# Kernel optimization log

Measured on AMD Instinct MI355X. Metric: run time of the kernel, lower is better.

Reference implementation:

```python
import jax, jax.numpy as jnp
import numpy as np

H = 12       # heads
D = 768      # hidden size
DH = D // H  # head dim = 64
SCALE = 1.0 / jnp.sqrt(jnp.float32(DH))
LN_EPS = 1e-3  # keras LayerNormalization default epsilon


def setup_inputs() -> dict:
    key = jax.random.key(0)
    ks = jax.random.split(key, 8)
    B, L = 16, 512
    s = 0.02  # truncated-normal-ish init scale
    return {
        "x": jax.random.normal(ks[0], (B, L, D), jnp.float32),
        "mask": jnp.ones((B, L), jnp.int32),
        "Wq": jax.random.normal(ks[1], (D, D), jnp.float32) * s,
        "bq": jnp.zeros((D,), jnp.float32),
        "Wk": jax.random.normal(ks[2], (D, D), jnp.float32) * s,
        "bk": jnp.zeros((D,), jnp.float32),
        "Wv": jax.random.normal(ks[3], (D, D), jnp.float32) * s,
        "bv": jnp.zeros((D,), jnp.float32),
        "Wo": jax.random.normal(ks[4], (D, D), jnp.float32) * s,
        "bo": jnp.zeros((D,), jnp.float32),
        "gamma": jnp.ones((D,), jnp.float32),
        "beta": jnp.zeros((D,), jnp.float32),
    }


def reference(x, mask, Wq, bq, Wk, bk, Wv, bv, Wo, bo, gamma, beta):
    B, L, _ = x.shape
    # QKV projections, split into heads: [B, L, H, DH]
    q = (x @ Wq + bq).reshape(B, L, H, DH)
    k = (x @ Wk + bk).reshape(B, L, H, DH)
    v = (x @ Wv + bv).reshape(B, L, H, DH)
    # scaled dot-product scores: [B, H, Lq, Lk]
    scores = jnp.einsum('bqhd,bkhd->bhqk', q, k) * SCALE
    # key-side padding mask (mask==0 -> -inf)
    neg = jnp.float32(-1e9)
    scores = jnp.where(mask[:, None, None, :] > 0, scores, neg)
    p = jax.nn.softmax(scores, axis=-1)
    # dropout rate fixed to 0.0 -> identity
    ctx = jnp.einsum('bhqk,bkhd->bqhd', p, v).reshape(B, L, D)
    attn_out = ctx @ Wo + bo
    # residual + LayerNorm (keras default eps=1e-3)
    y = x + attn_out
    mu = jnp.mean(y, axis=-1, keepdims=True)
    var = jnp.mean(jnp.square(y - mu), axis=-1, keepdims=True)
    return gamma * (y - mu) * jax.lax.rsqrt(var + LN_EPS) + beta
```

## Files before the change

### kernel.cpp

```cpp
#include <hip/hip_runtime.h>
#include <math.h>

#define NH 12
#define DMODEL 768
#define DHEAD 64
#define BATCH 16
#define SEQ 512
#define NTOK (BATCH*SEQ)
#define ATTN_SCALE 0.125f
#define LN_EPS 1e-3f
#define PADB 72
#define KITERS (DMODEL/64)

typedef __attribute__((ext_vector_type(8))) short  bf16x8;
typedef __attribute__((ext_vector_type(8))) unsigned short ushort8;
typedef __attribute__((ext_vector_type(4))) float  f32x4;

__device__ __forceinline__ unsigned short f2bf(float f) {
    unsigned int u = __float_as_uint(f);
    unsigned int r = (u + 0x7fffu + ((u >> 16) & 1u)) >> 16;
    return (unsigned short)r;
}
__device__ __forceinline__ float bf2f(unsigned short h) {
    return __uint_as_float(((unsigned int)h) << 16);
}

__device__ __forceinline__ void async_copy16(const void* g, void* l) {
    __builtin_amdgcn_global_load_lds((const __attribute__((address_space(1))) void*)g,
                                     (__attribute__((address_space(3))) void*)l,
                                     16, 0, 0);
}

__global__ __launch_bounds__(256) void prep_kernel(
    const float* __restrict__ x,
    const float* __restrict__ Wq, const float* __restrict__ Wk,
    const float* __restrict__ Wv, const float* __restrict__ Wo,
    unsigned short* __restrict__ xb,
    unsigned short* __restrict__ tq, unsigned short* __restrict__ tk,
    unsigned short* __restrict__ tv, unsigned short* __restrict__ to_)
{
    __shared__ float tile[32][33];
    const int bid = blockIdx.x;
    const int tid = threadIdx.x;

    if (bid < 6144) {
        int i = (bid * 256 + tid) * 4;
        const float4 v = *(const float4*)(x + i);
        unsigned long long pack =
              (unsigned long long)f2bf(v.x)
            | ((unsigned long long)f2bf(v.y) << 16)
            | ((unsigned long long)f2bf(v.z) << 32)
            | ((unsigned long long)f2bf(v.w) << 48);
        *(unsigned long long*)(xb + i) = pack;
        return;
    }

    const int t   = bid - 6144;
    const int zz  = t / 576;
    const int rem = t % 576;
    const float* W = (zz == 0) ? Wq : (zz == 1) ? Wk : (zz == 2) ? Wv : Wo;
    unsigned short* T = (zz == 0) ? tq : (zz == 1) ? tk : (zz == 2) ? tv : to_;

    const int bx = (rem / 24) * 32;
    const int by = (rem % 24) * 32;
    const int tx = tid & 31, ty = tid >> 5;

    #pragma unroll
    for (int i = 0; i < 32; i += 8)
        tile[ty + i][tx] = W[(size_t)(bx + ty + i) * DMODEL + by + tx];
    __syncthreads();
    #pragma unroll
    for (int i = 0; i < 32; i += 8)
        T[(size_t)(by + ty + i) * DMODEL + bx + tx] = f2bf(tile[tx][ty + i]);
}

__global__ __launch_bounds__(256, 4) void mfma_gemm_qkv(
    const unsigned short* __restrict__ xb,
    const unsigned short* __restrict__ wt0, const unsigned short* __restrict__ wt1,
    const unsigned short* __restrict__ wt2,
    const float* __restrict__ b0, const float* __restrict__ b1, const float* __restrict__ b2,
    unsigned short* __restrict__ o0, unsigned short* __restrict__ o1,
    unsigned short* __restrict__ o2)
{
    __shared__ __align__(16) unsigned short As[128 * 64];
    __shared__ __align__(16) unsigned short Bs[128 * 64];

    const int zz = blockIdx.z;
    const unsigned short* Wt = (zz == 0) ? wt0 : (zz == 1) ? wt1 : wt2;
    const float* bias        = (zz == 0) ? b0  : (zz == 1) ? b1  : b2;
    unsigned short* out      = (zz == 0) ? o0  : (zz == 1) ? o1  : o2;

    const int tid  = threadIdx.x;
    const int lane = tid & 63;
    const int w    = tid >> 6;
    const int wm   = w >> 1, wn = w & 1;
    const int m0   = blockIdx.x * 128;
    const int n0   = blockIdx.y * 128;
    const int quad = lane >> 4;
    const int l16  = lane & 15;

    const int rloc = lane >> 3;
    const int csw  = (lane & 7) ^ rloc;
    int rowS[4];
    #pragma unroll
    for (int ii = 0; ii < 4; ++ii) rowS[ii] = (4 * w + ii) * 8 + rloc;

    const int p0 = ((quad ^ (l16 & 7)) * 8);

    f32x4 acc[4][4] = {};

    for (int kb = 0; kb < KITERS; ++kb) {
        const int k0 = kb * 64;
        #pragma unroll
        for (int ii = 0; ii < 4; ++ii) {
            async_copy16(xb + (size_t)(m0 + rowS[ii]) * DMODEL + k0 + csw * 8,
                         As + (4 * w + ii) * 512);
            async_copy16(Wt + (size_t)(n0 + rowS[ii]) * DMODEL + k0 + csw * 8,
                         Bs + (4 * w + ii) * 512);
        }
        __syncthreads();

        #pragma unroll
        for (int ks = 0; ks < 2; ++ks) {
            const int po = p0 ^ (ks * 32);
            bf16x8 a[4], b[4];
            #pragma unroll
            for (int mi = 0; mi < 4; ++mi)
                a[mi] = *(const bf16x8*)&As[(wm * 64 + mi * 16 + l16) * 64 + po];
            #pragma unroll
            for (int ni = 0; ni < 4; ++ni)
                b[ni] = *(const bf16x8*)&Bs[(wn * 64 + ni * 16 + l16) * 64 + po];
            #pragma unroll
            for (int mi = 0; mi < 4; ++mi)
                #pragma unroll
                for (int ni = 0; ni < 4; ++ni)
                    acc[mi][ni] = __builtin_amdgcn_mfma_f32_16x16x32_bf16(a[mi], b[ni], acc[mi][ni], 0, 0, 0);
        }
        __syncthreads();
    }

    if (zz == 2) {
        #pragma unroll
        for (int ni = 0; ni < 4; ++ni) {
            const int ncol = n0 + wn * 64 + ni * 16 + l16;
            const int h = ncol >> 6, dh = ncol & 63;
            const float bv = bias[ncol];
            #pragma unroll
            for (int mi = 0; mi < 4; ++mi) {
                const int mbase = m0 + wm * 64 + mi * 16 + quad * 4;
                const int bi = mbase >> 9, l = mbase & 511;
                unsigned long long pack = 0;
                #pragma unroll
                for (int r = 0; r < 4; ++r)
                    pack |= (unsigned long long)f2bf(acc[mi][ni][r] + bv) << (16 * r);
                *(unsigned long long*)(out + ((size_t)((bi * NH + h) * DHEAD + dh)) * SEQ + l) = pack;
            }
        }
    } else {
        #pragma unroll
        for (int ni = 0; ni < 4; ++ni) {
            const int ncol = n0 + wn * 64 + ni * 16 + l16;
            const int h = ncol >> 6, dh = ncol & 63;
            const float bv = bias[ncol];
            #pragma unroll
            for (int mi = 0; mi < 4; ++mi) {
                const int mbase = m0 + wm * 64 + mi * 16 + quad * 4;
                #pragma unroll
                for (int r = 0; r < 4; ++r) {
                    const int t = mbase + r;
                    const int bi = t >> 9, l = t & 511;
                    out[(size_t)((bi * NH + h) * SEQ + l) * DHEAD + dh] = f2bf(acc[mi][ni][r] + bv);
                }
            }
        }
    }
}

__global__ __launch_bounds__(256, 4) void mfma_gemm_oproj(
    const unsigned short* __restrict__ ctxb, const unsigned short* __restrict__ wto,
    const float* __restrict__ bo, const float* __restrict__ x,
    float* __restrict__ y)
{
    __shared__ __align__(16) unsigned short As[128 * 64];
    __shared__ __align__(16) unsigned short Bs[128 * 64];

    const int tid  = threadIdx.x;
    const int lane = tid & 63;
    const int w    = tid >> 6;
    const int wm   = w >> 1, wn = w & 1;
    const int m0   = blockIdx.x * 128;
    const int n0   = blockIdx.y * 128;
    const int quad = lane >> 4;
    const int l16  = lane & 15;

    const int rloc = lane >> 3;
    const int csw  = (lane & 7) ^ rloc;
    int rowS[4];
    #pragma unroll
    for (int ii = 0; ii < 4; ++ii) rowS[ii] = (4 * w + ii) * 8 + rloc;
    const int p0 = ((quad ^ (l16 & 7)) * 8);

    f32x4 acc[4][4] = {};

    for (int kb = 0; kb < KITERS; ++kb) {
        const int k0 = kb * 64;
        #pragma unroll
        for (int ii = 0; ii < 4; ++ii) {
            async_copy16(ctxb + (size_t)(m0 + rowS[ii]) * DMODEL + k0 + csw * 8,
                         As + (4 * w + ii) * 512);
            async_copy16(wto  + (size_t)(n0 + rowS[ii]) * DMODEL + k0 + csw * 8,
                         Bs + (4 * w + ii) * 512);
        }
        __syncthreads();

        #pragma unroll
        for (int ks = 0; ks < 2; ++ks) {
            const int po = p0 ^ (ks * 32);
            bf16x8 a[4], b[4];
            #pragma unroll
            for (int mi = 0; mi < 4; ++mi)
                a[mi] = *(const bf16x8*)&As[(wm * 64 + mi * 16 + l16) * 64 + po];
            #pragma unroll
            for (int ni = 0; ni < 4; ++ni)
                b[ni] = *(const bf16x8*)&Bs[(wn * 64 + ni * 16 + l16) * 64 + po];
            #pragma unroll
            for (int mi = 0; mi < 4; ++mi)
                #pragma unroll
                for (int ni = 0; ni < 4; ++ni)
                    acc[mi][ni] = __builtin_amdgcn_mfma_f32_16x16x32_bf16(a[mi], b[ni], acc[mi][ni], 0, 0, 0);
        }
        __syncthreads();
    }

    #pragma unroll
    for (int ni = 0; ni < 4; ++ni) {
        const int ncol = n0 + wn * 64 + ni * 16 + l16;
        const float bv = bo[ncol];
        #pragma unroll
        for (int mi = 0; mi < 4; ++mi) {
            const int mbase = m0 + wm * 64 + mi * 16 + quad * 4;
            #pragma unroll
            for (int r = 0; r < 4; ++r) {
                const size_t idx = (size_t)(mbase + r) * DMODEL + ncol;
                y[idx] = acc[mi][ni][r] + bv + x[idx];
            }
        }
    }
}

__global__ __launch_bounds__(256) void attn_mfma_kernel(
    const unsigned short* __restrict__ q, const unsigned short* __restrict__ k,
    const unsigned short* __restrict__ vt, const int* __restrict__ mask,
    unsigned short* __restrict__ ctxb)
{
    __shared__ __align__(16) unsigned short Ks[64 * PADB];
    __shared__ __align__(16) unsigned short Vs[64 * PADB];
    __shared__ __align__(16) unsigned short QP[128 * PADB];
    __shared__ float maskF[64];

    const int tid  = threadIdx.x;
    const int lane = tid & 63;
    const int w    = tid >> 6;
    const int quad = lane >> 4;
    const int l16  = lane & 15;
    const int q0   = blockIdx.x * 128;
    const int h    = blockIdx.y;
    const int b    = blockIdx.z;

    const unsigned short* qp  = q  + ((size_t)(b * NH + h) * SEQ + q0) * DHEAD;
    const unsigned short* kp  = k  + (size_t)(b * NH + h) * SEQ * DHEAD;
    const unsigned short* vtp = vt + (size_t)(b * NH + h) * DHEAD * SEQ;

    #pragma unroll
    for (int i = 0; i < 4; ++i) {
        int idx = tid * 8 + 2048 * i;
        *(ushort8*)&QP[(idx >> 6) * PADB + (idx & 63)] = *(const ushort8*)(qp + idx);
    }
    __syncthreads();

    bf16x8 aQ[2][2];
    #pragma unroll
    for (int mi = 0; mi < 2; ++mi)
        #pragma unroll
        for (int kb = 0; kb < 2; ++kb)
            aQ[mi][kb] = *(const bf16x8*)&QP[(w * 32 + mi * 16 + l16) * PADB + kb * 32 + quad * 8];

    bf16x8 ones;
    #pragma unroll
    for (int j = 0; j < 8; ++j) ones[j] = (short)0x3F80;

    float m_st[2][4], l_st[2][4];
    #pragma unroll
    for (int mi = 0; mi < 2; ++mi)
        #pragma unroll
        for (int r = 0; r < 4; ++r) { m_st[mi][r] = -1e30f; l_st[mi][r] = 0.f; }
    f32x4 o[2][4] = {};
    const f32x4 zf = {0.f, 0.f, 0.f, 0.f};

    for (int kt = 0; kt < SEQ; kt += 64) {
        __syncthreads();
        #pragma unroll
        for (int i = 0; i < 2; ++i) {
            int idx = tid * 8 + 2048 * i;
            int r = idx >> 6, c = idx & 63;
            *(ushort8*)&Ks[r * PADB + c] = *(const ushort8*)(kp + (size_t)kt * DHEAD + idx);
            *(ushort8*)&Vs[r * PADB + c] = *(const ushort8*)(vtp + (size_t)r * SEQ + kt + c);
        }
        if (tid < 64) maskF[tid] = (mask[b * SEQ + kt + tid] > 0) ? 0.f : -1e9f;
        __syncthreads();

        f32x4 s[2][4];
        float mk[4];
        #pragma unroll
        for (int ni = 0; ni < 4; ++ni) {
            bf16x8 bK0 = *(const bf16x8*)&Ks[(ni * 16 + l16) * PADB + quad * 8];
            bf16x8 bK1 = *(const bf16x8*)&Ks[(ni * 16 + l16) * PADB + 32 + quad * 8];
            mk[ni] = maskF[ni * 16 + l16];
            #pragma unroll
            for (int mi = 0; mi < 2; ++mi) {
                f32x4 t0 = __builtin_amdgcn_mfma_f32_16x16x32_bf16(aQ[mi][0], bK0, zf, 0, 0, 0);
                s[mi][ni] = __builtin_amdgcn_mfma_f32_16x16x32_bf16(aQ[mi][1], bK1, t0, 0, 0, 0);
            }
        }

        float alpha[2][4];
        #pragma unroll
        for (int mi = 0; mi < 2; ++mi) {
            #pragma unroll
            for (int r = 0; r < 4; ++r) {
                float mx = -3e38f;
                #pragma unroll
                for (int ni = 0; ni < 4; ++ni) {
                    float sv = s[mi][ni][r] * ATTN_SCALE + mk[ni];
                    s[mi][ni][r] = sv;
                    mx = fmaxf(mx, sv);
                }
                mx = fmaxf(mx, __shfl_xor(mx, 1));
                mx = fmaxf(mx, __shfl_xor(mx, 2));
                mx = fmaxf(mx, __shfl_xor(mx, 4));
                mx = fmaxf(mx, __shfl_xor(mx, 8));
                float mo = m_st[mi][r];
                float mn = fmaxf(mo, mx);
                float al = __expf(mo - mn);
                m_st[mi][r] = mn;
                l_st[mi][r] *= al;
                alpha[mi][r] = al;
            }
        }

        #pragma unroll
        for (int mi = 0; mi < 2; ++mi)
            #pragma unroll
            for (int ni = 0; ni < 4; ++ni)
                #pragma unroll
                for (int r = 0; r < 4; ++r)
                    QP[(w * 32 + mi * 16 + quad * 4 + r) * PADB + ni * 16 + l16]
                        = f2bf(__expf(s[mi][ni][r] - m_st[mi][r]));
        #pragma unroll
        for (int mi = 0; mi < 2; ++mi)
            #pragma unroll
            for (int ni = 0; ni < 4; ++ni)
                #pragma unroll
                for (int r = 0; r < 4; ++r)
                    o[mi][ni][r] *= alpha[mi][r];

        bf16x8 aP[2][2];
        #pragma unroll
        for (int mi = 0; mi < 2; ++mi)
            #pragma unroll
            for (int kb = 0; kb < 2; ++kb)
                aP[mi][kb] = *(const bf16x8*)&QP[(w * 32 + mi * 16 + l16) * PADB + kb * 32 + quad * 8];

        f32x4 rs[2];
        #pragma unroll
        for (int mi = 0; mi < 2; ++mi) {
            f32x4 t0 = __builtin_amdgcn_mfma_f32_16x16x32_bf16(aP[mi][0], ones, zf, 0, 0, 0);
            rs[mi] = __builtin_amdgcn_mfma_f32_16x16x32_bf16(aP[mi][1], ones, t0, 0, 0, 0);
        }

        #pragma unroll
        for (int ni = 0; ni < 4; ++ni) {
            bf16x8 bV0 = *(const bf16x8*)&Vs[(ni * 16 + l16) * PADB + quad * 8];
            bf16x8 bV1 = *(const bf16x8*)&Vs[(ni * 16 + l16) * PADB + 32 + quad * 8];
            #pragma unroll
            for (int mi = 0; mi < 2; ++mi) {
                o[mi][ni] = __builtin_amdgcn_mfma_f32_16x16x32_bf16(aP[mi][0], bV0, o[mi][ni], 0, 0, 0);
                o[mi][ni] = __builtin_amdgcn_mfma_f32_16x16x32_bf16(aP[mi][1], bV1, o[mi][ni], 0, 0, 0);
            }
        }
        #pragma unroll
        for (int mi = 0; mi < 2; ++mi)
            #pragma unroll
            for (int r = 0; r < 4; ++r)
                l_st[mi][r] += rs[mi][r];
    }

    #pragma unroll
    for (int mi = 0; mi < 2; ++mi)
        #pragma unroll
        for (int r = 0; r < 4; ++r) {
            float inv = 1.f / l_st[mi][r];
            int tok = q0 + w * 32 + mi * 16 + quad * 4 + r;
            #pragma unroll
            for (int ni = 0; ni < 4; ++ni)
                ctxb[(size_t)(b * SEQ + tok) * DMODEL + h * DHEAD + ni * 16 + l16]
                    = f2bf(o[mi][ni][r] * inv);
        }
}

__global__ __launch_bounds__(256) void ln_kernel(
    const float* __restrict__ y, const float* __restrict__ gamma,
    const float* __restrict__ beta, float* __restrict__ out)
{
    const int t   = blockIdx.x;
    const int tid = threadIdx.x;
    const float* row = y + (size_t)t * DMODEL;

    float vals[3];
    float s = 0.f, s2 = 0.f;
    #pragma unroll
    for (int i = 0; i < 3; ++i) {
        float vv = row[tid + 256 * i];
        vals[i] = vv;
        s  += vv;
        s2 += vv * vv;
    }
    #pragma unroll
    for (int off = 32; off > 0; off >>= 1) {
        s  += __shfl_down(s,  off);
        s2 += __shfl_down(s2, off);
    }
    __shared__ float rbuf[8];
    int w = tid >> 6;
    if ((tid & 63) == 0) { rbuf[w] = s; rbuf[4 + w] = s2; }
    __syncthreads();
    float ts  = rbuf[0] + rbuf[1] + rbuf[2] + rbuf[3];
    float ts2 = rbuf[4] + rbuf[5] + rbuf[6] + rbuf[7];
    float mu  = ts * (1.f / DMODEL);
    float var = ts2 * (1.f / DMODEL) - mu * mu;
    float inv = rsqrtf(var + LN_EPS);
    #pragma unroll
    for (int i = 0; i < 3; ++i) {
        int c = tid + 256 * i;
        out[(size_t)t * DMODEL + c] = gamma[c] * (vals[i] - mu) * inv + beta[c];
    }
}

extern "C" void kernel_launch(void* const* d_in, const int* in_sizes, int n_in,
                              void* d_out, int out_size, void* d_ws, size_t ws_size,
                              hipStream_t stream) {
    const float* x     = (const float*)d_in[0];
    const int*   mask  = (const int*)  d_in[1];
    const float* Wq    = (const float*)d_in[2];
    const float* bq    = (const float*)d_in[3];
    const float* Wk    = (const float*)d_in[4];
    const float* bk    = (const float*)d_in[5];
    const float* Wv    = (const float*)d_in[6];
    const float* bv    = (const float*)d_in[7];
    const float* Wo    = (const float*)d_in[8];
    const float* bo    = (const float*)d_in[9];
    const float* gamma = (const float*)d_in[10];
    const float* beta  = (const float*)d_in[11];
    float* out = (float*)d_out;

    const size_t perTok = (size_t)NTOK * DMODEL;
    const size_t perW   = (size_t)DMODEL * DMODEL;

    unsigned short* xb   = (unsigned short*)d_ws;
    unsigned short* wtq  = xb + perTok;
    unsigned short* wtk  = wtq + perW;
    unsigned short* wtv  = wtk + perW;
    unsigned short* wto  = wtv + perW;
    unsigned short* qb   = wto + perW;
    unsigned short* kb   = qb + perTok;
    unsigned short* vb   = kb + perTok;
    unsigned short* ctxb = vb + perTok;
    float* y = out;

    prep_kernel<<<6144 + 2304, 256, 0, stream>>>(
        x, Wq, Wk, Wv, Wo, xb, wtq, wtk, wtv, wto);

    mfma_gemm_qkv<<<dim3(NTOK / 128, DMODEL / 128, 3), 256, 0, stream>>>(
        xb, wtq, wtk, wtv, bq, bk, bv, qb, kb, vb);

    attn_mfma_kernel<<<dim3(SEQ / 128, NH, BATCH), 256, 0, stream>>>(qb, kb, vb, mask, ctxb);

    mfma_gemm_oproj<<<dim3(NTOK / 128, DMODEL / 128), 256, 0, stream>>>(
        ctxb, wto, bo, x, y);

    ln_kernel<<<NTOK, 256, 0, stream>>>(y, gamma, beta, out);
}
```

Before: 217.2 us.

## Restructure attention: 64-query tiles, async swizzled LDS loads, folded scale, mask skip

```diff
diff --git a/kernel.cpp b/kernel.cpp
--- a/kernel.cpp
+++ b/kernel.cpp
@@ -9,7 +9,7 @@
 #define NTOK (BATCH*SEQ)
 #define ATTN_SCALE 0.125f
 #define LN_EPS 1e-3f
-#define PADB 72
+#define PADP 72
 #define KITERS (DMODEL/64)
 
 typedef __attribute__((ext_vector_type(8))) short  bf16x8;
@@ -20,9 +20,6 @@
     unsigned int u = __float_as_uint(f);
     unsigned int r = (u + 0x7fffu + ((u >> 16) & 1u)) >> 16;
     return (unsigned short)r;
-}
-__device__ __forceinline__ float bf2f(unsigned short h) {
-    return __uint_as_float(((unsigned int)h) << 16);
 }
 
 __device__ __forceinline__ void async_copy16(const void* g, void* l) {
@@ -89,6 +86,7 @@
     const unsigned short* Wt = (zz == 0) ? wt0 : (zz == 1) ? wt1 : wt2;
     const float* bias        = (zz == 0) ? b0  : (zz == 1) ? b1  : b2;
     unsigned short* out      = (zz == 0) ? o0  : (zz == 1) ? o1  : o2;
+    const float sc           = (zz == 0) ? ATTN_SCALE : 1.0f;
 
     const int tid  = threadIdx.x;
     const int lane = tid & 63;
@@ -169,7 +167,7 @@
                 for (int r = 0; r < 4; ++r) {
                     const int t = mbase + r;
                     const int bi = t >> 9, l = t & 511;
-                    out[(size_t)((bi * NH + h) * SEQ + l) * DHEAD + dh] = f2bf(acc[mi][ni][r] + bv);
+                    out[(size_t)((bi * NH + h) * SEQ + l) * DHEAD + dh] = f2bf((acc[mi][ni][r] + bv) * sc);
                 }
             }
         }
@@ -253,17 +251,19 @@
     const unsigned short* __restrict__ vt, const int* __restrict__ mask,
     unsigned short* __restrict__ ctxb)
 {
-    __shared__ __align__(16) unsigned short Ks[64 * PADB];
-    __shared__ __align__(16) unsigned short Vs[64 * PADB];
-    __shared__ __align__(16) unsigned short QP[128 * PADB];
+    __shared__ __align__(16) unsigned short Qs[64 * 64];
+    __shared__ __align__(16) unsigned short Ks[64 * 64];
+    __shared__ __align__(16) unsigned short Vs[64 * 64];
+    __shared__ __align__(16) unsigned short Ps[64 * PADP];
     __shared__ float maskF[64];
+    __shared__ int cleanS;
 
     const int tid  = threadIdx.x;
     const int lane = tid & 63;
     const int w    = tid >> 6;
     const int quad = lane >> 4;
     const int l16  = lane & 15;
-    const int q0   = blockIdx.x * 128;
+    const int q0   = blockIdx.x * 64;
     const int h    = blockIdx.y;
     const int b    = blockIdx.z;
 
@@ -271,141 +271,120 @@
     const unsigned short* kp  = k  + (size_t)(b * NH + h) * SEQ * DHEAD;
     const unsigned short* vtp = vt + (size_t)(b * NH + h) * DHEAD * SEQ;
 
-    #pragma unroll
-    for (int i = 0; i < 4; ++i) {
-        int idx = tid * 8 + 2048 * i;
-        *(ushort8*)&QP[(idx >> 6) * PADB + (idx & 63)] = *(const ushort8*)(qp + idx);
+    const int rloc = lane >> 3;
+    const int csw  = (lane & 7) ^ rloc;
+    const int p0   = (quad ^ (l16 & 7)) * 8;
+
+    #pragma unroll
+    for (int ii = 0; ii < 2; ++ii) {
+        const int inst = 2 * w + ii;
+        async_copy16(qp + (size_t)(inst * 8 + rloc) * DHEAD + csw * 8, Qs + inst * 512);
     }
     __syncthreads();
 
-    bf16x8 aQ[2][2];
-    #pragma unroll
-    for (int mi = 0; mi < 2; ++mi)
-        #pragma unroll
-        for (int kb = 0; kb < 2; ++kb)
-            aQ[mi][kb] = *(const bf16x8*)&QP[(w * 32 + mi * 16 + l16) * PADB + kb * 32 + quad * 8];
+    bf16x8 aQ[2];
+    #pragma unroll
+    for (int ks = 0; ks < 2; ++ks)
+        aQ[ks] = *(const bf16x8*)&Qs[(w * 16 + l16) * 64 + (p0 ^ (ks * 32))];
 
     bf16x8 ones;
     #pragma unroll
     for (int j = 0; j < 8; ++j) ones[j] = (short)0x3F80;
 
-    float m_st[2][4], l_st[2][4];
-    #pragma unroll
-    for (int mi = 0; mi < 2; ++mi)
-        #pragma unroll
-        for (int r = 0; r < 4; ++r) { m_st[mi][r] = -1e30f; l_st[mi][r] = 0.f; }
-    f32x4 o[2][4] = {};
+    float m_st[4], l_st[4];
+    #pragma unroll
+    for (int r = 0; r < 4; ++r) { m_st[r] = -1e30f; l_st[r] = 0.f; }
+    f32x4 o[4] = {};
     const f32x4 zf = {0.f, 0.f, 0.f, 0.f};
 
     for (int kt = 0; kt < SEQ; kt += 64) {
         __syncthreads();
         #pragma unroll
-        for (int i = 0; i < 2; ++i) {
-            int idx = tid * 8 + 2048 * i;
-            int r = idx >> 6, c = idx & 63;
-            *(ushort8*)&Ks[r * PADB + c] = *(const ushort8*)(kp + (size_t)kt * DHEAD + idx);
-            *(ushort8*)&Vs[r * PADB + c] = *(const ushort8*)(vtp + (size_t)r * SEQ + kt + c);
-        }
-        if (tid < 64) maskF[tid] = (mask[b * SEQ + kt + tid] > 0) ? 0.f : -1e9f;
-        __syncthreads();
-
-        f32x4 s[2][4];
-        float mk[4];
+        for (int ii = 0; ii < 2; ++ii) {
+            const int inst = 2 * w + ii;
+            async_copy16(kp  + (size_t)(kt + inst * 8 + rloc) * DHEAD + csw * 8, Ks + inst * 512);
+            async_copy16(vtp + (size_t)(inst * 8 + rloc) * SEQ + kt + csw * 8,   Vs + inst * 512);
+        }
+        if (tid < 64) {
+            const bool pm = mask[b * SEQ + kt + tid] > 0;
+            maskF[tid] = pm ? 0.f : -1e9f;
+            unsigned long long bb = __ballot(pm);
+            if (tid == 0) cleanS = (bb == 0xFFFFFFFFFFFFFFFFull) ? 1 : 0;
+        }
+        __syncthreads();
+
+        f32x4 s[4];
         #pragma unroll
         for (int ni = 0; ni < 4; ++ni) {
-            bf16x8 bK0 = *(const bf16x8*)&Ks[(ni * 16 + l16) * PADB + quad * 8];
-            bf16x8 bK1 = *(const bf16x8*)&Ks[(ni * 16 + l16) * PADB + 32 + quad * 8];
-            mk[ni] = maskF[ni * 16 + l16];
-            #pragma unroll
-            for (int mi = 0; mi < 2; ++mi) {
-                f32x4 t0 = __builtin_amdgcn_mfma_f32_16x16x32_bf16(aQ[mi][0], bK0, zf, 0, 0, 0);
-                s[mi][ni] = __builtin_amdgcn_mfma_f32_16x16x32_bf16(aQ[mi][1], bK1, t0, 0, 0, 0);
+            bf16x8 bK0 = *(const bf16x8*)&Ks[(ni * 16 + l16) * 64 + p0];
+            bf16x8 bK1 = *(const bf16x8*)&Ks[(ni * 16 + l16) * 64 + (p0 ^ 32)];
+            f32x4 t0 = __builtin_amdgcn_mfma_f32_16x16x32_bf16(aQ[0], bK0, zf, 0, 0, 0);
+            s[ni] = __builtin_amdgcn_mfma_f32_16x16x32_bf16(aQ[1], bK1, t0, 0, 0, 0);
+        }
+        if (cleanS == 0) {
+            #pragma unroll
+            for (int ni = 0; ni < 4; ++ni) {
+                const float mk = maskF[ni * 16 + l16];
+                #pragma unroll
+                for (int r = 0; r < 4; ++r) s[ni][r] += mk;
             }
         }
 
-        float alpha[2][4];
-        #pragma unroll
-        for (int mi = 0; mi < 2; ++mi) {
-            #pragma unroll
-            for (int r = 0; r < 4; ++r) {
-                float mx = -3e38f;
-                #pragma unroll
-                for (int ni = 0; ni < 4; ++ni) {
-                    float sv = s[mi][ni][r] * ATTN_SCALE + mk[ni];
-                    s[mi][ni][r] = sv;
-                    mx = fmaxf(mx, sv);
-                }
-                mx = fmaxf(mx, __shfl_xor(mx, 1));
-                mx = fmaxf(mx, __shfl_xor(mx, 2));
-                mx = fmaxf(mx, __shfl_xor(mx, 4));
-                mx = fmaxf(mx, __shfl_xor(mx, 8));
-                float mo = m_st[mi][r];
-                float mn = fmaxf(mo, mx);
-                float al = __expf(mo - mn);
-                m_st[mi][r] = mn;
-                l_st[mi][r] *= al;
-                alpha[mi][r] = al;
-            }
-        }
-
-        #pragma unroll
-        for (int mi = 0; mi < 2; ++mi)
-            #pragma unroll
-            for (int ni = 0; ni < 4; ++ni)
-                #pragma unroll
-                for (int r = 0; r < 4; ++r)
-                    QP[(w * 32 + mi * 16 + quad * 4 + r) * PADB + ni * 16 + l16]
-                        = f2bf(__expf(s[mi][ni][r] - m_st[mi][r]));
-        #pragma unroll
-        for (int mi = 0; mi < 2; ++mi)
-            #pragma unroll
-            for (int ni = 0; ni < 4; ++ni)
-                #pragma unroll
-                for (int r = 0; r < 4; ++r)
-                    o[mi][ni][r] *= alpha[mi][r];
-
-        bf16x8 aP[2][2];
-        #pragma unroll
-        for (int mi = 0; mi < 2; ++mi)
-            #pragma unroll
-            for (int kb = 0; kb < 2; ++kb)
-                aP[mi][kb] = *(const bf16x8*)&QP[(w * 32 + mi * 16 + l16) * PADB + kb * 32 + quad * 8];
-
-        f32x4 rs[2];
-        #pragma unroll
-        for (int mi = 0; mi < 2; ++mi) {
-            f32x4 t0 = __builtin_amdgcn_mfma_f32_16x16x32_bf16(aP[mi][0], ones, zf, 0, 0, 0);
-            rs[mi] = __builtin_amdgcn_mfma_f32_16x16x32_bf16(aP[mi][1], ones, t0, 0, 0, 0);
-        }
+        float alpha[4];
+        #pragma unroll
+        for (int r = 0; r < 4; ++r) {
+            float mx = fmaxf(fmaxf(s[0][r], s[1][r]), fmaxf(s[2][r], s[3][r]));
+            mx = fmaxf(mx, __shfl_xor(mx, 1));
+            mx = fmaxf(mx, __shfl_xor(mx, 2));
+            mx = fmaxf(mx, __shfl_xor(mx, 4));
+            mx = fmaxf(mx, __shfl_xor(mx, 8));
+            const float mo = m_st[r];
+            const float mn = fmaxf(mo, mx);
+            alpha[r] = __expf(mo - mn);
+            m_st[r] = mn;
+            l_st[r] *= alpha[r];
+        }
+
+        #pragma unroll
+        for (int ni = 0; ni < 4; ++ni)
+            #pragma unroll
+            for (int r = 0; r < 4; ++r)
+                Ps[(w * 16 + quad * 4 + r) * PADP + ni * 16 + l16]
+                    = f2bf(__expf(s[ni][r] - m_st[r]));
+        #pragma unroll
+        for (int ni = 0; ni < 4; ++ni)
+            #pragma unroll
+            for (int r = 0; r < 4; ++r)
+                o[ni][r] *= alpha[r];
+
+        bf16x8 aP[2];
+        #pragma unroll
+        for (int ks = 0; ks < 2; ++ks)
+            aP[ks] = *(const bf16x8*)&Ps[(w * 16 + l16) * PADP + quad * 8 + ks * 32];
+
+        f32x4 t0 = __builtin_amdgcn_mfma_f32_16x16x32_bf16(aP[0], ones, zf, 0, 0, 0);
+        f32x4 rs = __builtin_amdgcn_mfma_f32_16x16x32_bf16(aP[1], ones, t0, 0, 0, 0);
 
         #pragma unroll
         for (int ni = 0; ni < 4; ++ni) {
-            bf16x8 bV0 = *(const bf16x8*)&Vs[(ni * 16 + l16) * PADB + quad * 8];
-            bf16x8 bV1 = *(const bf16x8*)&Vs[(ni * 16 + l16) * PADB + 32 + quad * 8];
-            #pragma unroll
-            for (int mi = 0; mi < 2; ++mi) {
-                o[mi][ni] = __builtin_amdgcn_mfma_f32_16x16x32_bf16(aP[mi][0], bV0, o[mi][ni], 0, 0, 0);
-                o[mi][ni] = __builtin_amdgcn_mfma_f32_16x16x32_bf16(aP[mi][1], bV1, o[mi][ni], 0, 0, 0);
-            }
-        }
-        #pragma unroll
-        for (int mi = 0; mi < 2; ++mi)
-            #pragma unroll
-            for (int r = 0; r < 4; ++r)
-                l_st[mi][r] += rs[mi][r];
-    }
-
-    #pragma unroll
-    for (int mi = 0; mi < 2; ++mi)
-        #pragma unroll
-        for (int r = 0; r < 4; ++r) {
-            float inv = 1.f / l_st[mi][r];
-            int tok = q0 + w * 32 + mi * 16 + quad * 4 + r;
-            #pragma unroll
-            for (int ni = 0; ni < 4; ++ni)
-                ctxb[(size_t)(b * SEQ + tok) * DMODEL + h * DHEAD + ni * 16 + l16]
-                    = f2bf(o[mi][ni][r] * inv);
-        }
+            bf16x8 bV0 = *(const bf16x8*)&Vs[(ni * 16 + l16) * 64 + p0];
+            bf16x8 bV1 = *(const bf16x8*)&Vs[(ni * 16 + l16) * 64 + (p0 ^ 32)];
+            o[ni] = __builtin_amdgcn_mfma_f32_16x16x32_bf16(aP[0], bV0, o[ni], 0, 0, 0);
+            o[ni] = __builtin_amdgcn_mfma_f32_16x16x32_bf16(aP[1], bV1, o[ni], 0, 0, 0);
+        }
+        #pragma unroll
+        for (int r = 0; r < 4; ++r) l_st[r] += rs[r];
+    }
+
+    #pragma unroll
+    for (int r = 0; r < 4; ++r) {
+        const float inv = 1.f / l_st[r];
+        const int tok = q0 + w * 16 + quad * 4 + r;
+        #pragma unroll
+        for (int ni = 0; ni < 4; ++ni)
+            ctxb[(size_t)(b * SEQ + tok) * DMODEL + h * DHEAD + ni * 16 + l16]
+                = f2bf(o[ni][r] * inv);
+    }
 }
 
 __global__ __launch_bounds__(256) void ln_kernel(
@@ -483,7 +462,7 @@
     mfma_gemm_qkv<<<dim3(NTOK / 128, DMODEL / 128, 3), 256, 0, stream>>>(
         xb, wtq, wtk, wtv, bq, bk, bv, qb, kb, vb);
 
-    attn_mfma_kernel<<<dim3(SEQ / 128, NH, BATCH), 256, 0, stream>>>(qb, kb, vb, mask, ctxb);
+    attn_mfma_kernel<<<dim3(SEQ / 64, NH, BATCH), 256, 0, stream>>>(qb, kb, vb, mask, ctxb);
 
     mfma_gemm_oproj<<<dim3(NTOK / 128, DMODEL / 128), 256, 0, stream>>>(
         ctxb, wto, bo, x, y);
```

Measured after the change: 214.2 us. About the same (-1.4%).
